# Kernel tuning notes

Hardware: AMD Instinct MI355X
Metric: run time of the kernel (lower is better)

Reference implementation:

```python
import jax, jax.numpy as jnp
import numpy as np

B, S, D = 4, 2048, 512
H, DK, DV = 8, 64, 64


def setup_inputs() -> dict:
    key = jax.random.key(0)
    ks = jax.random.split(key, 12)
    inv = 1.0 / np.sqrt(D)
    return {
        "query": jax.random.normal(ks[0], (B, S, D), dtype=jnp.float32),
        "value": jax.random.normal(ks[1], (B, S, D), dtype=jnp.float32),
        "attention_mask": jax.random.randint(ks[2], (B, S), 0, 2, dtype=jnp.int32),
        "Wq": jax.random.normal(ks[3], (D, H * DK), dtype=jnp.float32) * inv,
        "bq": jnp.zeros((H * DK,), dtype=jnp.float32),
        "Wk": jax.random.normal(ks[4], (D, H * DK), dtype=jnp.float32) * inv,
        "bk": jnp.zeros((H * DK,), dtype=jnp.float32),
        "Wv": jax.random.normal(ks[5], (D, H * DV), dtype=jnp.float32) * inv,
        "bv": jnp.zeros((H * DV,), dtype=jnp.float32),
        "Wo": jax.random.normal(ks[6], (H * DV, D), dtype=jnp.float32) * inv,
        "bo": jnp.zeros((D,), dtype=jnp.float32),
    }


def _split_heads(x, h):
    b, s, _ = x.shape
    return x.reshape(b, s, h, -1).transpose(0, 2, 1, 3)  # (B,H,S,dh)


def reference(query, value, attention_mask, Wq, bq, Wk, bk, Wv, bv, Wo, bo):
    # QKV projections (activation=None -> identity); key defaults to value
    q = _split_heads(query @ Wq + bq, H)   # (B,H,S,DK)
    k = _split_heads(value @ Wk + bk, H)   # (B,H,S,DK)
    v = _split_heads(value @ Wv + bv, H)   # (B,H,S,DV)

    scores = jnp.einsum("bhqd,bhkd->bhqk", q, k) / jnp.sqrt(jnp.float32(DK))
    # additive mask: m = 1e9*(mask-1), applied on both key and query axes
    m = 1e9 * (attention_mask.astype(jnp.float32) - 1.0)  # (B,S)
    scores = scores + m[:, None, None, :] + m[:, None, :, None]

    weights = jax.nn.softmax(scores, axis=-1)
    ctx = jnp.einsum("bhqk,bhkd->bhqd", weights, v)        # (B,H,S,DV)
    ctx = ctx.transpose(0, 2, 1, 3).reshape(ctx.shape[0], ctx.shape[2], H * DV)
    return ctx @ Wo + bo  # (B,S,D)
```

## Files before the change

### kernel.cpp

```cpp
#include <hip/hip_runtime.h>

#define B_ 4
#define S_ 2048
#define D_ 512
#define H_ 8

typedef __attribute__((ext_vector_type(8))) __bf16 bf16x8;
typedef __attribute__((ext_vector_type(4))) float f32x4;

#define NEGBIG  -1.442695040e9f
#define QSCALE  0.18033688011112042f

__device__ __forceinline__ unsigned pack_rn(float a, float b) {
    union { float f; unsigned u; } ua, ub; ua.f = a; ub.f = b;
    return __builtin_amdgcn_perm(ub.u + 0x8000u, ua.u + 0x8000u, 0x07060302u);
}

__global__ __launch_bounds__(256) void cast_x(
    const float* __restrict__ q, const float* __restrict__ v,
    unsigned short* __restrict__ xq, unsigned short* __restrict__ xv)
{
    const float* src = blockIdx.z ? v : q;
    unsigned short* dst = blockIdx.z ? xv : xq;
    int i = (blockIdx.x * 256 + threadIdx.x) * 8;
    float4 f0 = *(const float4*)&src[i];
    float4 f1 = *(const float4*)&src[i + 4];
    uint4 o;
    o.x = pack_rn(f0.x, f0.y); o.y = pack_rn(f0.z, f0.w);
    o.z = pack_rn(f1.x, f1.y); o.w = pack_rn(f1.z, f1.w);
    *(uint4*)&dst[i] = o;
}

__global__ __launch_bounds__(256) void compact_k(
    const int* __restrict__ am, int* __restrict__ idxc, int* __restrict__ nv1)
{
    const int w = threadIdx.x >> 6;
    const int lane = threadIdx.x & 63;
    const int* amb = am + w * 2048;
    int* ib = idxc + w * 2048;
    const unsigned long long ltmask = (1ULL << lane) - 1ULL;
    int base = 0;
    for (int step = 0; step < 32; ++step) {
        int s = step * 64 + lane;
        int m = amb[s];
        unsigned long long bal = __ballot(m != 0);
        if (m) ib[base + __popcll(bal & ltmask)] = s;
        base += __popcll(bal);
    }
    if (lane == 0) nv1[w] = base;
}

__global__ __launch_bounds__(256) void mask_fc(
    const int* __restrict__ am, const int* __restrict__ nv1,
    float* __restrict__ Mf, float* __restrict__ Mc, int* __restrict__ nv2)
{
    int g = (blockIdx.x * 256 + threadIdx.x) * 4;
    int b = g >> 11, loc = g & 2047;
    int nv = nv1[b];
    int4 m = *(const int4*)&am[g];
    float4 o, c;
    o.x = m.x ? 0.f : NEGBIG;
    o.y = m.y ? 0.f : NEGBIG;
    o.z = m.z ? 0.f : NEGBIG;
    o.w = m.w ? 0.f : NEGBIG;
    c.x = (loc + 0 < nv) ? 0.f : NEGBIG;
    c.y = (loc + 1 < nv) ? 0.f : NEGBIG;
    c.z = (loc + 2 < nv) ? 0.f : NEGBIG;
    c.w = (loc + 3 < nv) ? 0.f : NEGBIG;
    *(float4*)&Mf[g] = o;
    *(float4*)&Mc[g] = c;
    if (blockIdx.x == 0 && threadIdx.x < 4) nv2[threadIdx.x] = nv1[threadIdx.x];
}

__global__ __launch_bounds__(256) void cast_wt(
    const float* __restrict__ Wq, const float* __restrict__ Wk,
    const float* __restrict__ Wv, const float* __restrict__ Wo,
    unsigned short* __restrict__ Tq, unsigned short* __restrict__ Tk,
    unsigned short* __restrict__ Tv, unsigned short* __restrict__ To)
{
    int z = blockIdx.z;
    const float* W = (z == 0) ? Wq : (z == 1) ? Wk : (z == 2) ? Wv : Wo;
    unsigned short* T = (z == 0) ? Tq : (z == 1) ? Tk : (z == 2) ? Tv : To;
    int n0 = blockIdx.x * 64, k0 = blockIdx.y * 64;
    int tid = threadIdx.x;

    __shared__ float Ts[64][69];
    #pragma unroll
    for (int it = 0; it < 4; it++) {
        int lin = tid + it * 256;
        int kr = lin >> 4, c4 = (lin & 15) * 4;
        float4 v = *(const float4*)&W[(k0 + kr) * 512 + n0 + c4];
        Ts[kr][c4 + 0] = v.x; Ts[kr][c4 + 1] = v.y;
        Ts[kr][c4 + 2] = v.z; Ts[kr][c4 + 3] = v.w;
    }
    __syncthreads();
    int n = tid >> 2, kc = tid & 3;
    unsigned p[8];
    #pragma unroll
    for (int j = 0; j < 8; j++)
        p[j] = pack_rn(Ts[kc * 16 + 2 * j][n], Ts[kc * 16 + 2 * j + 1][n]);
    unsigned short* dst = &T[(n0 + n) * 512 + k0 + kc * 16];
    *(uint4*)dst       = *(uint4*)&p[0];
    *(uint4*)(dst + 8) = *(uint4*)&p[4];
}

__global__ __launch_bounds__(256) void proj_qkv_mfma(
    const unsigned short* __restrict__ Xq, const unsigned short* __restrict__ Xv,
    const unsigned short* __restrict__ Wtq, const unsigned short* __restrict__ Wtk,
    const unsigned short* __restrict__ Wtv,
    const float* __restrict__ bq, const float* __restrict__ bk,
    const float* __restrict__ bv,
    const int* __restrict__ idxc, const int* __restrict__ nv1,
    unsigned short* __restrict__ Qb, unsigned short* __restrict__ Kb,
    unsigned short* __restrict__ VtG)
{
    const int z = blockIdx.z;
    const unsigned short* A  = (z == 0) ? Wtq : (z == 1) ? Wtk : Xv;
    const unsigned short* Bm = (z == 0) ? Xq  : (z == 1) ? Xv  : Wtv;
    const float* bias        = (z == 0) ? bq  : (z == 1) ? bk  : bv;
    const int m0 = (z < 2) ? blockIdx.y * 128 : blockIdx.x * 128;
    const int n0 = (z < 2) ? blockIdx.x * 128 : blockIdx.y * 128;

    if (z == 1) {
        int bb = n0 >> 11, cap = (nv1[bb] + 127) & ~127;
        if (cap < 128) cap = 128;
        if ((n0 & 2047) >= cap) return;
    }
    if (z == 2) {
        int bb = m0 >> 11, cap = (nv1[bb] + 127) & ~127;
        if (cap < 128) cap = 128;
        if ((m0 & 2047) >= cap) return;
    }

    const int tid = threadIdx.x;
    const int w = tid >> 6, lane = tid & 63;
    const int l15 = lane & 15, quad = lane >> 4;
    const int wm = (w >> 1) * 64, wn = (w & 1) * 64;

    __shared__ unsigned short As[128 * 72];
    __shared__ unsigned short Bs[128 * 72];

    long aoff[2], boff[2];
    bool az[2] = {false, false}, bz[2] = {false, false};
    #pragma unroll
    for (int it = 0; it < 2; it++) {
        int row = (tid + it * 256) >> 2;
        long sa = m0 + row, sb = n0 + row;
        if (z == 2) {
            int bb = (m0 + row) >> 11, loc = (m0 + row) & 2047;
            if (loc < nv1[bb]) sa = bb * 2048 + idxc[bb * 2048 + loc];
            else az[it] = true;
        }
        if (z == 1) {
            int bb = (n0 + row) >> 11, loc = (n0 + row) & 2047;
            if (loc < nv1[bb]) sb = bb * 2048 + idxc[bb * 2048 + loc];
            else bz[it] = true;
        }
        aoff[it] = sa * 512; boff[it] = sb * 512;
    }

    f32x4 acc[4][4];
    #pragma unroll
    for (int i = 0; i < 4; i++)
        #pragma unroll
        for (int j = 0; j < 4; j++) acc[i][j] = (f32x4){0.f, 0.f, 0.f, 0.f};

    const uint4 zero4 = {0u, 0u, 0u, 0u};
    for (int k0 = 0; k0 < 512; k0 += 64) {
        __syncthreads();
        #pragma unroll
        for (int it = 0; it < 2; it++) {
            int lin = tid + it * 256;
            int row = lin >> 2, c2 = (lin & 3) * 2;
            uint4 a0 = az[it] ? zero4 : *(const uint4*)&A[aoff[it] + k0 + c2 * 8];
            uint4 a1 = az[it] ? zero4 : *(const uint4*)&A[aoff[it] + k0 + c2 * 8 + 8];
            uint4 b0 = bz[it] ? zero4 : *(const uint4*)&Bm[boff[it] + k0 + c2 * 8];
            uint4 b1 = bz[it] ? zero4 : *(const uint4*)&Bm[boff[it] + k0 + c2 * 8 + 8];
            *(uint4*)&As[row * 72 + c2 * 8]     = a0;
            *(uint4*)&As[row * 72 + c2 * 8 + 8] = a1;
            *(uint4*)&Bs[row * 72 + c2 * 8]     = b0;
            *(uint4*)&Bs[row * 72 + c2 * 8 + 8] = b1;
        }
        __syncthreads();
        #pragma unroll
        for (int kc = 0; kc < 2; kc++) {
            bf16x8 a[4], bb[4];
            #pragma unroll
            for (int i = 0; i < 4; i++)
                a[i] = *(const bf16x8*)&As[(wm + 16 * i + l15) * 72 + kc * 32 + quad * 8];
            #pragma unroll
            for (int j = 0; j < 4; j++)
                bb[j] = *(const bf16x8*)&Bs[(wn + 16 * j + l15) * 72 + kc * 32 + quad * 8];
            #pragma unroll
            for (int i = 0; i < 4; i++)
                #pragma unroll
                for (int j = 0; j < 4; j++)
                    acc[i][j] = __builtin_amdgcn_mfma_f32_16x16x32_bf16(a[i], bb[j], acc[i][j], 0, 0, 0);
        }
    }

    if (z == 2) {
        #pragma unroll
        for (int j = 0; j < 4; j++) {
            int N = n0 + wn + 16 * j + l15;
            float bv_ = bias[N];
            int h = N >> 6, d = N & 63;
            #pragma unroll
            for (int i = 0; i < 4; i++) {
                int Mb = m0 + wm + 16 * i + quad * 4;
                int b = Mb >> 11, s = Mb & 2047;
                uint2 o;
                o.x = pack_rn(acc[i][j][0] + bv_, acc[i][j][1] + bv_);
                o.y = pack_rn(acc[i][j][2] + bv_, acc[i][j][3] + bv_);
                *(uint2*)&VtG[((b * H_ + h) * 64 + d) * 2048 + s] = o;
            }
        }
    } else {
        unsigned short* dst = (z == 0) ? Qb : Kb;
        const float scale = (z == 0) ? QSCALE : 1.0f;
        #pragma unroll
        for (int j = 0; j < 4; j++) {
            int sg = n0 + wn + 16 * j + l15;
            int b = sg >> 11, s = sg & 2047;
            #pragma unroll
            for (int i = 0; i < 4; i++) {
                int F = m0 + wm + 16 * i + quad * 4;
                int h = F >> 6, d = F & 63;
                float4 b4 = *(const float4*)&bias[F];
                uint2 o;
                o.x = pack_rn((acc[i][j][0] + b4.x) * scale, (acc[i][j][1] + b4.y) * scale);
                o.y = pack_rn((acc[i][j][2] + b4.z) * scale, (acc[i][j][3] + b4.w) * scale);
                *(uint2*)&dst[((b * H_ + h) * 2048 + s) * 64 + d] = o;
            }
        }
    }
}

__global__ __launch_bounds__(256, 2) void flash_mfma(
    const unsigned short* __restrict__ Qg, const unsigned short* __restrict__ Kg,
    const unsigned short* __restrict__ VtG, const float* __restrict__ Mf,
    const float* __restrict__ Mc, const int* __restrict__ nvalid,
    unsigned short* __restrict__ ctxB)
{
    const int bid = blockIdx.x;
    const int xcd = bid & 7, idx = bid >> 3;
    const int bh = xcd * 4 + (idx & 3);
    const int q0 = (idx >> 2) * 128;
    const int b = bh >> 3, h = bh & 7;

    const int tid = threadIdx.x;
    const int w = tid >> 6, lane = tid & 63;
    const int l15 = lane & 15, quad = lane >> 4;
    const int swz = l15 & 7;

    __shared__ unsigned short Ks[2][64 * 64];
    __shared__ unsigned short Ps[4][32 * 64];
    unsigned short* pw = &Ps[w][0];

    const int nv = nvalid[b];
    int ntiles = (nv + 63) >> 6;
    if (ntiles < 1) ntiles = 1;

    const float* mfb = Mf + b * 2048;
    const float* mcp = Mc + b * 2048 + quad * 4;

    bf16x8 qf[2][2];
    float mq[2];
    #pragma unroll
    for (int qb = 0; qb < 2; qb++) {
        int qrow = q0 + w * 32 + qb * 16 + l15;
        const unsigned short* p = &Qg[((long)bh * 2048 + qrow) * 64 + quad * 8];
        qf[qb][0] = *(const bf16x8*)p;
        qf[qb][1] = *(const bf16x8*)(p + 32);
        mq[qb] = mfb[qrow];
    }

    const unsigned short* vp[4];
    #pragma unroll
    for (int i = 0; i < 4; i++)
        vp[i] = VtG + ((long)bh * 64 + i * 16 + l15) * 2048 + quad * 8;

    const int srow = tid >> 2;
    const int sch  = (tid & 3) * 2;
    const unsigned short* kgb = Kg + (long)bh * 2048 * 64;
    const int sw0 = srow * 64 + ((sch    ) ^ (srow & 7)) * 8;
    const int sw1 = srow * 64 + ((sch + 1) ^ (srow & 7)) * 8;

    {
        uint4 a = *(const uint4*)&kgb[srow * 64 + sch * 8];
        uint4 c = *(const uint4*)&kgb[srow * 64 + sch * 8 + 8];
        *(uint4*)&Ks[0][sw0] = a;
        *(uint4*)&Ks[0][sw1] = c;
    }

    const int koff0 = ((quad    ) ^ swz) * 8;
    const int koff1 = ((quad + 4) ^ swz) * 8;

    f32x4 accO[2][4];
    #pragma unroll
    for (int qb = 0; qb < 2; qb++)
        #pragma unroll
        for (int dt = 0; dt < 4; dt++) accO[qb][dt] = (f32x4){0.f, 0.f, 0.f, 0.f};
    float mi[2] = {-3.0e38f, -3.0e38f};
    float li[2] = {0.f, 0.f};

    __syncthreads();

    for (int t = 0; t < ntiles; t++) {
        const int kt = t * 64;
        const int ktn = (t + 1 < ntiles) ? kt + 64 : kt;
        const int cur = t & 1, nxt = cur ^ 1;

        bf16x8 vf[4][2];
        #pragma unroll
        for (int dt = 0; dt < 4; dt++) {
            vf[dt][0] = *(const bf16x8*)(vp[dt] + kt);
            vf[dt][1] = *(const bf16x8*)(vp[dt] + kt + 32);
        }
        uint4 kst0 = *(const uint4*)&kgb[(ktn + srow) * 64 + sch * 8];
        uint4 kst1 = *(const uint4*)&kgb[(ktn + srow) * 64 + sch * 8 + 8];
        f32x4 kmf[4];
        #pragma unroll
        for (int nt = 0; nt < 4; nt++)
            kmf[nt] = *(const f32x4*)(mcp + kt + nt * 16);

        bf16x8 kf[4][2];
        #pragma unroll
        for (int nt = 0; nt < 4; nt++) {
            kf[nt][0] = *(const bf16x8*)&Ks[cur][(nt * 16 + l15) * 64 + koff0];
            kf[nt][1] = *(const bf16x8*)&Ks[cur][(nt * 16 + l15) * 64 + koff1];
        }
        f32x4 sc[2][4];
        #pragma unroll
        for (int qb = 0; qb < 2; qb++)
            #pragma unroll
            for (int nt = 0; nt < 4; nt++) {
                f32x4 c = kmf[nt];
                c[0] += mq[qb]; c[1] += mq[qb]; c[2] += mq[qb]; c[3] += mq[qb];
                sc[qb][nt] = c;
            }
        __builtin_amdgcn_s_setprio(1);
        #pragma unroll
        for (int qb = 0; qb < 2; qb++)
            #pragma unroll
            for (int nt = 0; nt < 4; nt++) {
                sc[qb][nt] = __builtin_amdgcn_mfma_f32_16x16x32_bf16(
                    kf[nt][0], qf[qb][0], sc[qb][nt], 0, 0, 0);
                sc[qb][nt] = __builtin_amdgcn_mfma_f32_16x16x32_bf16(
                    kf[nt][1], qf[qb][1], sc[qb][nt], 0, 0, 0);
            }
        __builtin_amdgcn_s_setprio(0);

        #pragma unroll
        for (int qb = 0; qb < 2; qb++) {
            float mloc = fmaxf(fmaxf(sc[qb][0][0], sc[qb][0][1]),
                               fmaxf(sc[qb][0][2], sc[qb][0][3]));
            #pragma unroll
            for (int nt = 1; nt < 4; nt++)
                mloc = fmaxf(mloc, fmaxf(fmaxf(sc[qb][nt][0], sc[qb][nt][1]),
                                         fmaxf(sc[qb][nt][2], sc[qb][nt][3])));
            mloc = fmaxf(mloc, __shfl_xor(mloc, 16));
            mloc = fmaxf(mloc, __shfl_xor(mloc, 32));

            float mn = mi[qb];
            if (!__all(mloc <= mn + 4.f)) {
                float mo = mn;
                mn = fmaxf(mo, mloc);
                float alpha = __builtin_amdgcn_exp2f(mo - mn);
                li[qb] *= alpha;
                #pragma unroll
                for (int dt = 0; dt < 4; dt++) {
                    accO[qb][dt][0] *= alpha; accO[qb][dt][1] *= alpha;
                    accO[qb][dt][2] *= alpha; accO[qb][dt][3] *= alpha;
                }
                mi[qb] = mn;
            }

            float ps = 0.f;
            const int prbase = (qb * 16 + l15) * 64;
            #pragma unroll
            for (int nt = 0; nt < 4; nt++) {
                float p0 = __builtin_amdgcn_exp2f(sc[qb][nt][0] - mn);
                float p1 = __builtin_amdgcn_exp2f(sc[qb][nt][1] - mn);
                float p2 = __builtin_amdgcn_exp2f(sc[qb][nt][2] - mn);
                float p3 = __builtin_amdgcn_exp2f(sc[qb][nt][3] - mn);
                ps += (p0 + p1) + (p2 + p3);
                uint2 pp;
                pp.x = pack_rn(p0, p1);
                pp.y = pack_rn(p2, p3);
                *(uint2*)&pw[prbase + ((2 * nt + (quad >> 1)) ^ swz) * 8 + (quad & 1) * 4] = pp;
            }
            ps += __shfl_xor(ps, 16);
            ps += __shfl_xor(ps, 32);
            li[qb] += ps;
        }

        #pragma unroll
        for (int qb = 0; qb < 2; qb++) {
            bf16x8 pf0 = *(const bf16x8*)&pw[(qb * 16 + l15) * 64 + koff0];
            bf16x8 pf1 = *(const bf16x8*)&pw[(qb * 16 + l15) * 64 + koff1];
            __builtin_amdgcn_s_setprio(1);
            #pragma unroll
            for (int dt = 0; dt < 4; dt++) {
                accO[qb][dt] = __builtin_amdgcn_mfma_f32_16x16x32_bf16(
                    vf[dt][0], pf0, accO[qb][dt], 0, 0, 0);
                accO[qb][dt] = __builtin_amdgcn_mfma_f32_16x16x32_bf16(
                    vf[dt][1], pf1, accO[qb][dt], 0, 0, 0);
            }
            __builtin_amdgcn_s_setprio(0);
        }

        *(uint4*)&Ks[nxt][sw0] = kst0;
        *(uint4*)&Ks[nxt][sw1] = kst1;
        __syncthreads();
    }

    #pragma unroll
    for (int qb = 0; qb < 2; qb++) {
        float inv = 1.f / li[qb];
        int q = q0 + w * 32 + qb * 16 + l15;
        int obase = (b * 2048 + q) * 512 + h * 64 + quad * 4;
        #pragma unroll
        for (int dt = 0; dt < 4; dt++) {
            uint2 o;
            o.x = pack_rn(accO[qb][dt][0] * inv, accO[qb][dt][1] * inv);
            o.y = pack_rn(accO[qb][dt][2] * inv, accO[qb][dt][3] * inv);
            *(uint2*)&ctxB[obase + dt * 16] = o;
        }
    }
}

__global__ __launch_bounds__(256) void proj_out_mfma(
    const unsigned short* __restrict__ ctxB, const unsigned short* __restrict__ Wto,
    const float* __restrict__ bo, float* __restrict__ out)
{
    const int m0 = blockIdx.y * 128, n0 = blockIdx.x * 128;
    const int tid = threadIdx.x;
    const int w = tid >> 6, lane = tid & 63;
    const int l15 = lane & 15, quad = lane >> 4;
    const int wm = (w >> 1) * 64, wn = (w & 1) * 64;

    __shared__ unsigned short As[128 * 72];
    __shared__ unsigned short Bs[128 * 72];

    f32x4 acc[4][4];
    #pragma unroll
    for (int i = 0; i < 4; i++)
        #pragma unroll
        for (int j = 0; j < 4; j++) acc[i][j] = (f32x4){0.f, 0.f, 0.f, 0.f};

    for (int k0 = 0; k0 < 512; k0 += 64) {
        __syncthreads();
        #pragma unroll
        for (int it = 0; it < 2; it++) {
            int lin = tid + it * 256;
            int row = lin >> 2, c2 = (lin & 3) * 2;
            *(uint4*)&As[row * 72 + c2 * 8]     = *(const uint4*)&Wto[(m0 + row) * 512 + k0 + c2 * 8];
            *(uint4*)&As[row * 72 + c2 * 8 + 8] = *(const uint4*)&Wto[(m0 + row) * 512 + k0 + c2 * 8 + 8];
            *(uint4*)&Bs[row * 72 + c2 * 8]     = *(const uint4*)&ctxB[(n0 + row) * 512 + k0 + c2 * 8];
            *(uint4*)&Bs[row * 72 + c2 * 8 + 8] = *(const uint4*)&ctxB[(n0 + row) * 512 + k0 + c2 * 8 + 8];
        }
        __syncthreads();
        #pragma unroll
        for (int kc = 0; kc < 2; kc++) {
            bf16x8 a[4], bb[4];
            #pragma unroll
            for (int i = 0; i < 4; i++)
                a[i] = *(const bf16x8*)&As[(wm + 16 * i + l15) * 72 + kc * 32 + quad * 8];
            #pragma unroll
            for (int j = 0; j < 4; j++)
                bb[j] = *(const bf16x8*)&Bs[(wn + 16 * j + l15) * 72 + kc * 32 + quad * 8];
            #pragma unroll
            for (int i = 0; i < 4; i++)
                #pragma unroll
                for (int j = 0; j < 4; j++)
                    acc[i][j] = __builtin_amdgcn_mfma_f32_16x16x32_bf16(a[i], bb[j], acc[i][j], 0, 0, 0);
        }
    }

    #pragma unroll
    for (int j = 0; j < 4; j++) {
        int sg = n0 + wn + 16 * j + l15;
        #pragma unroll
        for (int i = 0; i < 4; i++) {
            int F = m0 + wm + 16 * i + quad * 4;
            float4 b4 = *(const float4*)&bo[F];
            float4 vv;
            vv.x = acc[i][j][0] + b4.x;
            vv.y = acc[i][j][1] + b4.y;
            vv.z = acc[i][j][2] + b4.z;
            vv.w = acc[i][j][3] + b4.w;
            *(float4*)&out[sg * 512 + F] = vv;
        }
    }
}

extern "C" void kernel_launch(void* const* d_in, const int* in_sizes, int n_in,
                              void* d_out, int out_size, void* d_ws, size_t ws_size,
                              hipStream_t stream)
{
    const float* query = (const float*)d_in[0];
    const float* value = (const float*)d_in[1];
    const int*   amask = (const int*)d_in[2];
    const float* Wq = (const float*)d_in[3];
    const float* bq = (const float*)d_in[4];
    const float* Wk = (const float*)d_in[5];
    const float* bk = (const float*)d_in[6];
    const float* Wv = (const float*)d_in[7];
    const float* bv = (const float*)d_in[8];
    const float* Wo = (const float*)d_in[9];
    const float* bo = (const float*)d_in[10];
    float* out = (float*)d_out;

    char* ws = (char*)d_ws;
    const size_t MB = 1 << 20;
    const size_t KB = 1 << 10;
    unsigned short* Xbq = (unsigned short*)(ws);
    unsigned short* Xbv = (unsigned short*)(ws + 8 * MB);
    unsigned short* Wtq = (unsigned short*)(ws + 16 * MB);
    unsigned short* Wtk = (unsigned short*)(ws + 16 * MB + MB / 2);
    unsigned short* Wtv = (unsigned short*)(ws + 17 * MB);
    unsigned short* Wto = (unsigned short*)(ws + 17 * MB + MB / 2);
    unsigned short* Qb  = (unsigned short*)(ws + 18 * MB);
    unsigned short* Kb  = (unsigned short*)(ws + 26 * MB);
    unsigned short* VtG = (unsigned short*)(ws + 34 * MB);
    unsigned short* ctx = (unsigned short*)(ws + 42 * MB);

    int*   idx1 = (int*)(ws + 42 * MB);
    int*   nv1  = (int*)(ws + 42 * MB + 32 * KB);
    float* Mf   = (float*)(ws);
    float* Mc   = (float*)(ws + 32 * KB);
    int*   nv2  = (int*)(ws + 64 * KB);

    cast_x<<<dim3(2048, 1, 2), 256, 0, stream>>>(query, value, Xbq, Xbv);
    cast_wt<<<dim3(8, 8, 4), 256, 0, stream>>>(Wq, Wk, Wv, Wo, Wtq, Wtk, Wtv, Wto);
    compact_k<<<dim3(1), 256, 0, stream>>>(amask, idx1, nv1);
    proj_qkv_mfma<<<dim3(64, 4, 3), 256, 0, stream>>>(Xbq, Xbv, Wtq, Wtk, Wtv,
                                                      bq, bk, bv, idx1, nv1,
                                                      Qb, Kb, VtG);
    mask_fc<<<dim3(8), 256, 0, stream>>>(amask, nv1, Mf, Mc, nv2);
    flash_mfma<<<dim3(512), 256, 0, stream>>>(Qb, Kb, VtG, Mf, Mc, nv2, ctx);
    proj_out_mfma<<<dim3(64, 4), 256, 0, stream>>>(ctx, Wto, bo, out);
}
```

Measured before the change: 212.6 us.

## Fuse preprocessing kernels and use direct global-to-LDS loads with XOR swizzle

Merges the input cast, weight transpose-cast, mask compaction and mask-fill kernels into one launch, cutting four prologue kernels down to one. Both projection GEMMs now stage tiles with global_load_lds 16-byte direct copies into an XOR-swizzled unpadded LDS layout instead of register round-trips with padding. Masked padding rows are handled by zero-filling the compaction index tail rather than per-load predication, so padded rows read real data from row 0. The ctx buffer is aliased onto the query cast buffer to reuse workspace.

After: 187.6 us. -11.8%, faster.

```diff
diff --git a/kernel.cpp b/kernel.cpp
--- a/kernel.cpp
+++ b/kernel.cpp
@@ -16,92 +16,90 @@
     return __builtin_amdgcn_perm(ub.u + 0x8000u, ua.u + 0x8000u, 0x07060302u);
 }
 
-__global__ __launch_bounds__(256) void cast_x(
+__device__ __forceinline__ void gl16(const void* g, void* l) {
+    __builtin_amdgcn_global_load_lds(
+        (const __attribute__((address_space(1))) unsigned int*)g,
+        (__attribute__((address_space(3))) unsigned int*)l, 16, 0, 0);
+}
+
+__global__ __launch_bounds__(256) void pre_all(
     const float* __restrict__ q, const float* __restrict__ v,
-    unsigned short* __restrict__ xq, unsigned short* __restrict__ xv)
-{
-    const float* src = blockIdx.z ? v : q;
-    unsigned short* dst = blockIdx.z ? xv : xq;
-    int i = (blockIdx.x * 256 + threadIdx.x) * 8;
-    float4 f0 = *(const float4*)&src[i];
-    float4 f1 = *(const float4*)&src[i + 4];
-    uint4 o;
-    o.x = pack_rn(f0.x, f0.y); o.y = pack_rn(f0.z, f0.w);
-    o.z = pack_rn(f1.x, f1.y); o.w = pack_rn(f1.z, f1.w);
-    *(uint4*)&dst[i] = o;
-}
-
-__global__ __launch_bounds__(256) void compact_k(
-    const int* __restrict__ am, int* __restrict__ idxc, int* __restrict__ nv1)
-{
-    const int w = threadIdx.x >> 6;
-    const int lane = threadIdx.x & 63;
-    const int* amb = am + w * 2048;
-    int* ib = idxc + w * 2048;
-    const unsigned long long ltmask = (1ULL << lane) - 1ULL;
-    int base = 0;
-    for (int step = 0; step < 32; ++step) {
-        int s = step * 64 + lane;
-        int m = amb[s];
-        unsigned long long bal = __ballot(m != 0);
-        if (m) ib[base + __popcll(bal & ltmask)] = s;
-        base += __popcll(bal);
-    }
-    if (lane == 0) nv1[w] = base;
-}
-
-__global__ __launch_bounds__(256) void mask_fc(
-    const int* __restrict__ am, const int* __restrict__ nv1,
-    float* __restrict__ Mf, float* __restrict__ Mc, int* __restrict__ nv2)
-{
-    int g = (blockIdx.x * 256 + threadIdx.x) * 4;
-    int b = g >> 11, loc = g & 2047;
-    int nv = nv1[b];
-    int4 m = *(const int4*)&am[g];
-    float4 o, c;
-    o.x = m.x ? 0.f : NEGBIG;
-    o.y = m.y ? 0.f : NEGBIG;
-    o.z = m.z ? 0.f : NEGBIG;
-    o.w = m.w ? 0.f : NEGBIG;
-    c.x = (loc + 0 < nv) ? 0.f : NEGBIG;
-    c.y = (loc + 1 < nv) ? 0.f : NEGBIG;
-    c.z = (loc + 2 < nv) ? 0.f : NEGBIG;
-    c.w = (loc + 3 < nv) ? 0.f : NEGBIG;
-    *(float4*)&Mf[g] = o;
-    *(float4*)&Mc[g] = c;
-    if (blockIdx.x == 0 && threadIdx.x < 4) nv2[threadIdx.x] = nv1[threadIdx.x];
-}
-
-__global__ __launch_bounds__(256) void cast_wt(
+    const int* __restrict__ am,
     const float* __restrict__ Wq, const float* __restrict__ Wk,
     const float* __restrict__ Wv, const float* __restrict__ Wo,
+    unsigned short* __restrict__ xq, unsigned short* __restrict__ xv,
     unsigned short* __restrict__ Tq, unsigned short* __restrict__ Tk,
-    unsigned short* __restrict__ Tv, unsigned short* __restrict__ To)
+    unsigned short* __restrict__ Tv, unsigned short* __restrict__ To,
+    int* __restrict__ idxc, int* __restrict__ nvout,
+    float* __restrict__ Mf, float* __restrict__ Mc)
 {
-    int z = blockIdx.z;
-    const float* W = (z == 0) ? Wq : (z == 1) ? Wk : (z == 2) ? Wv : Wo;
-    unsigned short* T = (z == 0) ? Tq : (z == 1) ? Tk : (z == 2) ? Tv : To;
-    int n0 = blockIdx.x * 64, k0 = blockIdx.y * 64;
-    int tid = threadIdx.x;
-
-    __shared__ float Ts[64][69];
-    #pragma unroll
-    for (int it = 0; it < 4; it++) {
-        int lin = tid + it * 256;
-        int kr = lin >> 4, c4 = (lin & 15) * 4;
-        float4 v = *(const float4*)&W[(k0 + kr) * 512 + n0 + c4];
-        Ts[kr][c4 + 0] = v.x; Ts[kr][c4 + 1] = v.y;
-        Ts[kr][c4 + 2] = v.z; Ts[kr][c4 + 3] = v.w;
-    }
-    __syncthreads();
-    int n = tid >> 2, kc = tid & 3;
-    unsigned p[8];
-    #pragma unroll
-    for (int j = 0; j < 8; j++)
-        p[j] = pack_rn(Ts[kc * 16 + 2 * j][n], Ts[kc * 16 + 2 * j + 1][n]);
-    unsigned short* dst = &T[(n0 + n) * 512 + k0 + kc * 16];
-    *(uint4*)dst       = *(uint4*)&p[0];
-    *(uint4*)(dst + 8) = *(uint4*)&p[4];
+    const int bid = blockIdx.x;
+    const int tid = threadIdx.x;
+
+    if (bid < 4096) {
+        const int z = bid >> 11, xb = bid & 2047;
+        const float* src = z ? v : q;
+        unsigned short* dst = z ? xv : xq;
+        int i = (xb * 256 + tid) * 8;
+        float4 f0 = *(const float4*)&src[i];
+        float4 f1 = *(const float4*)&src[i + 4];
+        uint4 o;
+        o.x = pack_rn(f0.x, f0.y); o.y = pack_rn(f0.z, f0.w);
+        o.z = pack_rn(f1.x, f1.y); o.w = pack_rn(f1.z, f1.w);
+        *(uint4*)&dst[i] = o;
+    } else if (bid < 4352) {
+        int r = bid - 4096;
+        int z = r >> 6, rem = r & 63;
+        const float* W = (z == 0) ? Wq : (z == 1) ? Wk : (z == 2) ? Wv : Wo;
+        unsigned short* T = (z == 0) ? Tq : (z == 1) ? Tk : (z == 2) ? Tv : To;
+        int n0 = (rem & 7) * 64, k0 = (rem >> 3) * 64;
+
+        __shared__ float Ts[64][69];
+        #pragma unroll
+        for (int it = 0; it < 4; it++) {
+            int lin = tid + it * 256;
+            int kr = lin >> 4, c4 = (lin & 15) * 4;
+            float4 vv = *(const float4*)&W[(k0 + kr) * 512 + n0 + c4];
+            Ts[kr][c4 + 0] = vv.x; Ts[kr][c4 + 1] = vv.y;
+            Ts[kr][c4 + 2] = vv.z; Ts[kr][c4 + 3] = vv.w;
+        }
+        __syncthreads();
+        int n = tid >> 2, kc = tid & 3;
+        unsigned p[8];
+        #pragma unroll
+        for (int j = 0; j < 8; j++)
+            p[j] = pack_rn(Ts[kc * 16 + 2 * j][n], Ts[kc * 16 + 2 * j + 1][n]);
+        unsigned short* dst = &T[(n0 + n) * 512 + k0 + kc * 16];
+        *(uint4*)dst       = *(uint4*)&p[0];
+        *(uint4*)(dst + 8) = *(uint4*)&p[4];
+    } else {
+        const int w = tid >> 6, lane = tid & 63;
+        const int* amb = am + w * 2048;
+        int m[32];
+        #pragma unroll
+        for (int s = 0; s < 32; s++) m[s] = amb[s * 64 + lane];
+
+        int* ib = idxc + w * 2048;
+        const unsigned long long lt = (1ULL << lane) - 1ULL;
+        int base = 0;
+        #pragma unroll
+        for (int s = 0; s < 32; s++) {
+            unsigned long long bal = __ballot(m[s] != 0);
+            if (m[s]) ib[base + __popcll(bal & lt)] = s * 64 + lane;
+            base += __popcll(bal);
+        }
+        const int nv = base;
+        for (int i = nv + lane; i < 2048; i += 64) ib[i] = 0;
+        float* mfb = Mf + w * 2048;
+        float* mcb = Mc + w * 2048;
+        #pragma unroll
+        for (int s = 0; s < 32; s++) {
+            int i = s * 64 + lane;
+            mfb[i] = m[s] ? 0.f : NEGBIG;
+            mcb[i] = (i < nv) ? 0.f : NEGBIG;
+        }
+        if (lane == 0) nvout[w] = nv;
+    }
 }
 
 __global__ __launch_bounds__(256) void proj_qkv_mfma(
@@ -137,27 +135,30 @@
     const int l15 = lane & 15, quad = lane >> 4;
     const int wm = (w >> 1) * 64, wn = (w & 1) * 64;
 
-    __shared__ unsigned short As[128 * 72];
-    __shared__ unsigned short Bs[128 * 72];
-
-    long aoff[2], boff[2];
-    bool az[2] = {false, false}, bz[2] = {false, false};
-    #pragma unroll
-    for (int it = 0; it < 2; it++) {
-        int row = (tid + it * 256) >> 2;
-        long sa = m0 + row, sb = n0 + row;
-        if (z == 2) {
-            int bb = (m0 + row) >> 11, loc = (m0 + row) & 2047;
-            if (loc < nv1[bb]) sa = bb * 2048 + idxc[bb * 2048 + loc];
-            else az[it] = true;
-        }
-        if (z == 1) {
-            int bb = (n0 + row) >> 11, loc = (n0 + row) & 2047;
-            if (loc < nv1[bb]) sb = bb * 2048 + idxc[bb * 2048 + loc];
-            else bz[it] = true;
-        }
-        aoff[it] = sa * 512; boff[it] = sb * 512;
-    }
+    __shared__ unsigned short As[128 * 64];
+    __shared__ unsigned short Bs[128 * 64];
+
+    const int srw  = tid >> 3;
+    const int csrc = (tid & 7) ^ (srw & 7);
+    const unsigned short* aS[4];
+    const unsigned short* bS[4];
+    unsigned short* la[4];
+    unsigned short* lb[4];
+    #pragma unroll
+    for (int is = 0; is < 4; is++) {
+        int ra = m0 + is * 32 + srw;
+        int rb = n0 + is * 32 + srw;
+        long sa = ra, sb = rb;
+        if (z == 2) { int bb = ra >> 11; sa = (long)bb * 2048 + idxc[bb * 2048 + (ra & 2047)]; }
+        if (z == 1) { int bb = rb >> 11; sb = (long)bb * 2048 + idxc[bb * 2048 + (rb & 2047)]; }
+        aS[is] = A  + sa * 512 + csrc * 8;
+        bS[is] = Bm + sb * 512 + csrc * 8;
+        la[is] = &As[is * 2048 + w * 512];
+        lb[is] = &Bs[is * 2048 + w * 512];
+    }
+
+    const int koff0 = ((quad    ) ^ (l15 & 7)) * 8;
+    const int koff1 = ((quad + 4) ^ (l15 & 7)) * 8;
 
     f32x4 acc[4][4];
     #pragma unroll
@@ -165,32 +166,24 @@
         #pragma unroll
         for (int j = 0; j < 4; j++) acc[i][j] = (f32x4){0.f, 0.f, 0.f, 0.f};
 
-    const uint4 zero4 = {0u, 0u, 0u, 0u};
     for (int k0 = 0; k0 < 512; k0 += 64) {
         __syncthreads();
         #pragma unroll
-        for (int it = 0; it < 2; it++) {
-            int lin = tid + it * 256;
-            int row = lin >> 2, c2 = (lin & 3) * 2;
-            uint4 a0 = az[it] ? zero4 : *(const uint4*)&A[aoff[it] + k0 + c2 * 8];
-            uint4 a1 = az[it] ? zero4 : *(const uint4*)&A[aoff[it] + k0 + c2 * 8 + 8];
-            uint4 b0 = bz[it] ? zero4 : *(const uint4*)&Bm[boff[it] + k0 + c2 * 8];
-            uint4 b1 = bz[it] ? zero4 : *(const uint4*)&Bm[boff[it] + k0 + c2 * 8 + 8];
-            *(uint4*)&As[row * 72 + c2 * 8]     = a0;
-            *(uint4*)&As[row * 72 + c2 * 8 + 8] = a1;
-            *(uint4*)&Bs[row * 72 + c2 * 8]     = b0;
-            *(uint4*)&Bs[row * 72 + c2 * 8 + 8] = b1;
+        for (int is = 0; is < 4; is++) {
+            gl16(aS[is] + k0, la[is]);
+            gl16(bS[is] + k0, lb[is]);
         }
         __syncthreads();
         #pragma unroll
         for (int kc = 0; kc < 2; kc++) {
+            const int ko = kc ? koff1 : koff0;
             bf16x8 a[4], bb[4];
             #pragma unroll
             for (int i = 0; i < 4; i++)
-                a[i] = *(const bf16x8*)&As[(wm + 16 * i + l15) * 72 + kc * 32 + quad * 8];
+                a[i] = *(const bf16x8*)&As[(wm + 16 * i + l15) * 64 + ko];
             #pragma unroll
             for (int j = 0; j < 4; j++)
-                bb[j] = *(const bf16x8*)&Bs[(wn + 16 * j + l15) * 72 + kc * 32 + quad * 8];
+                bb[j] = *(const bf16x8*)&Bs[(wn + 16 * j + l15) * 64 + ko];
             #pragma unroll
             for (int i = 0; i < 4; i++)
                 #pragma unroll
@@ -440,8 +433,24 @@
     const int l15 = lane & 15, quad = lane >> 4;
     const int wm = (w >> 1) * 64, wn = (w & 1) * 64;
 
-    __shared__ unsigned short As[128 * 72];
-    __shared__ unsigned short Bs[128 * 72];
+    __shared__ unsigned short As[128 * 64];
+    __shared__ unsigned short Bs[128 * 64];
+
+    const int srw  = tid >> 3;
+    const int csrc = (tid & 7) ^ (srw & 7);
+    const unsigned short* aS[4];
+    const unsigned short* bS[4];
+    unsigned short* la[4];
+    unsigned short* lb[4];
+    #pragma unroll
+    for (int is = 0; is < 4; is++) {
+        aS[is] = Wto  + (long)(m0 + is * 32 + srw) * 512 + csrc * 8;
+        bS[is] = ctxB + (long)(n0 + is * 32 + srw) * 512 + csrc * 8;
+        la[is] = &As[is * 2048 + w * 512];
+        lb[is] = &Bs[is * 2048 + w * 512];
+    }
+    const int koff0 = ((quad    ) ^ (l15 & 7)) * 8;
+    const int koff1 = ((quad + 4) ^ (l15 & 7)) * 8;
 
     f32x4 acc[4][4];
     #pragma unroll
@@ -452,24 +461,21 @@
     for (int k0 = 0; k0 < 512; k0 += 64) {
         __syncthreads();
         #pragma unroll
-        for (int it = 0; it < 2; it++) {
-            int lin = tid + it * 256;
-            int row = lin >> 2, c2 = (lin & 3) * 2;
-            *(uint4*)&As[row * 72 + c2 * 8]     = *(const uint4*)&Wto[(m0 + row) * 512 + k0 + c2 * 8];
-            *(uint4*)&As[row * 72 + c2 * 8 + 8] = *(const uint4*)&Wto[(m0 + row) * 512 + k0 + c2 * 8 + 8];
-            *(uint4*)&Bs[row * 72 + c2 * 8]     = *(const uint4*)&ctxB[(n0 + row) * 512 + k0 + c2 * 8];
-            *(uint4*)&Bs[row * 72 + c2 * 8 + 8] = *(const uint4*)&ctxB[(n0 + row) * 512 + k0 + c2 * 8 + 8];
+        for (int is = 0; is < 4; is++) {
+            gl16(aS[is] + k0, la[is]);
+            gl16(bS[is] + k0, lb[is]);
         }
         __syncthreads();
         #pragma unroll
         for (int kc = 0; kc < 2; kc++) {
+            const int ko = kc ? koff1 : koff0;
             bf16x8 a[4], bb[4];
             #pragma unroll
             for (int i = 0; i < 4; i++)
-                a[i] = *(const bf16x8*)&As[(wm + 16 * i + l15) * 72 + kc * 32 + quad * 8];
+                a[i] = *(const bf16x8*)&As[(wm + 16 * i + l15) * 64 + ko];
             #pragma unroll
             for (int j = 0; j < 4; j++)
-                bb[j] = *(const bf16x8*)&Bs[(wn + 16 * j + l15) * 72 + kc * 32 + quad * 8];
+                bb[j] = *(const bf16x8*)&Bs[(wn + 16 * j + l15) * 64 + ko];
             #pragma unroll
             for (int i = 0; i < 4; i++)
                 #pragma unroll
@@ -524,21 +530,19 @@
     unsigned short* Qb  = (unsigned short*)(ws + 18 * MB);
     unsigned short* Kb  = (unsigned short*)(ws + 26 * MB);
     unsigned short* VtG = (unsigned short*)(ws + 34 * MB);
-    unsigned short* ctx = (unsigned short*)(ws + 42 * MB);
-
     int*   idx1 = (int*)(ws + 42 * MB);
-    int*   nv1  = (int*)(ws + 42 * MB + 32 * KB);
-    float* Mf   = (float*)(ws);
-    float* Mc   = (float*)(ws + 32 * KB);
-    int*   nv2  = (int*)(ws + 64 * KB);
-
-    cast_x<<<dim3(2048, 1, 2), 256, 0, stream>>>(query, value, Xbq, Xbv);
-    cast_wt<<<dim3(8, 8, 4), 256, 0, stream>>>(Wq, Wk, Wv, Wo, Wtq, Wtk, Wtv, Wto);
-    compact_k<<<dim3(1), 256, 0, stream>>>(amask, idx1, nv1);
+    float* Mf   = (float*)(ws + 42 * MB + 32 * KB);
+    float* Mc   = (float*)(ws + 42 * MB + 64 * KB);
+    int*   nv   = (int*)(ws + 42 * MB + 96 * KB);
+    unsigned short* ctx = Xbq;
+
+    pre_all<<<dim3(4353), 256, 0, stream>>>(query, value, amask,
+                                            Wq, Wk, Wv, Wo,
+                                            Xbq, Xbv, Wtq, Wtk, Wtv, Wto,
+                                            idx1, nv, Mf, Mc);
     proj_qkv_mfma<<<dim3(64, 4, 3), 256, 0, stream>>>(Xbq, Xbv, Wtq, Wtk, Wtv,
-                                                      bq, bk, bv, idx1, nv1,
+                                                      bq, bk, bv, idx1, nv,
                                                       Qb, Kb, VtG);
-    mask_fc<<<dim3(8), 256, 0, stream>>>(amask, nv1, Mf, Mc, nv2);
-    flash_mfma<<<dim3(512), 256, 0, stream>>>(Qb, Kb, VtG, Mf, Mc, nv2, ctx);
+    flash_mfma<<<dim3(512), 256, 0, stream>>>(Qb, Kb, VtG, Mf, Mc, nv, ctx);
     proj_out_mfma<<<dim3(64, 4), 256, 0, stream>>>(ctx, Wto, bo, out);
 }
```
